# Kernel optimization log

Hardware: AMD Instinct MI355X
Metric: run time of the kernel (lower is better)

The kernel has to match this reference:

```python
import jax, jax.numpy as jnp
import numpy as np

EMBED_DIM = 1024
NUM_HEADS = 16
HEAD_DIM = EMBED_DIM // NUM_HEADS


def setup_inputs() -> dict:
    key = jax.random.key(0)
    ks = jax.random.split(key, 8)
    B, S, D = 4, 2048, EMBED_DIM
    scale = 1.0 / np.sqrt(D)
    return {
        "values": jax.random.normal(ks[0], (B, S, D), jnp.float32),
        "keys": jax.random.normal(ks[1], (B, S, D), jnp.float32),
        "query": jax.random.normal(ks[2], (B, S, D), jnp.float32),
        "Wv": jax.random.normal(ks[3], (D, D), jnp.float32) * scale,
        "Wk": jax.random.normal(ks[4], (D, D), jnp.float32) * scale,
        "Wq": jax.random.normal(ks[5], (D, D), jnp.float32) * scale,
        "Wo": jax.random.normal(ks[6], (D, D), jnp.float32) * scale,
        "bo": jnp.zeros((D,), jnp.float32),
    }


def reference(values, keys, query, Wv, Wk, Wq, Wo, bo):
    N = query.shape[0]
    H, Dh = NUM_HEADS, HEAD_DIM
    # torch Linear: x @ W.T  (weights stored [out, in])
    v = (values @ Wv.T).reshape(N, -1, H, Dh)
    k = (keys @ Wk.T).reshape(N, -1, H, Dh)
    q = (query @ Wq.T).reshape(N, -1, H, Dh)
    # energy: [N, H, q, k]
    energy = jnp.einsum("nqhd,nkhd->nhqk", q, k)
    # NOTE: original scales by sqrt(embed_dim), not sqrt(head_dim)
    attn = jax.nn.softmax(energy / jnp.sqrt(jnp.float32(EMBED_DIM)), axis=3)
    out = jnp.einsum("nhql,nlhd->nqhd", attn, v).reshape(N, -1, H * Dh)
    return out @ Wo.T + bo
```

## Files before the change

### kernel.cpp

```cpp
#include <hip/hip_runtime.h>
#include <stdint.h>

#define S_LEN   2048
#define D_MODEL 1024
#define N_HEADS 16
#define D_HEAD  64
#define BATCH   4
#define GM      8192
#define GN      1024
#define GK      1024
#define NKT     16

typedef __attribute__((ext_vector_type(8)))  short short8;
typedef __attribute__((ext_vector_type(4)))  short short4v;
typedef __attribute__((ext_vector_type(4)))  float f32x4;
typedef __attribute__((ext_vector_type(16))) float f32x16;

__device__ __forceinline__ short f2bf(float f) {
  unsigned u = __builtin_bit_cast(unsigned, f);
  u += 0x7fffu + ((u >> 16) & 1u);
  return (short)(u >> 16);
}

__device__ __forceinline__ unsigned cvt_pk_bf16(float lo, float hi) {
  unsigned r;
  asm("v_cvt_pk_bf16_f32 %0, %1, %2" : "=v"(r) : "v"(lo), "v"(hi));
  return r;
}

__device__ __forceinline__ short8 cvtf8(const float4 f0, const float4 f1) {
  unsigned u[4] = { cvt_pk_bf16(f0.x, f0.y), cvt_pk_bf16(f0.z, f0.w),
                    cvt_pk_bf16(f1.x, f1.y), cvt_pk_bf16(f1.z, f1.w) };
  return __builtin_bit_cast(short8, *(ulonglong2*)u);
}

__device__ __forceinline__ void gload_lds16(const short* g, short* lds_base) {
  __builtin_amdgcn_global_load_lds(
      (const __attribute__((address_space(1))) void*)(const void*)g,
      (__attribute__((address_space(3))) void*)(void*)lds_base, 16, 0, 0);
}

__global__ __launch_bounds__(256)
void cast_w(const float* __restrict__ W0, const float* __restrict__ W1,
            const float* __restrict__ W2, const float* __restrict__ W3,
            short* __restrict__ O0, short* __restrict__ O1,
            short* __restrict__ O2, short* __restrict__ O3)
{
  const int y = blockIdx.y;
  const float* src = (y == 0) ? W0 : (y == 1) ? W1 : (y == 2) ? W2 : W3;
  short*       dst = (y == 0) ? O0 : (y == 1) ? O1 : (y == 2) ? O2 : O3;
  const int gid = blockIdx.x * 256 + threadIdx.x;
  const int row = gid >> 7, gr = gid & 127;
  const int og  = (gr & ~7) | ((gr & 7) ^ (row & 7));
  const float* p = src + row * 1024 + gr * 8;
  short8 v = cvtf8(*(const float4*)p, *(const float4*)(p + 4));
  *(short8*)(dst + row * 1024 + og * 8) = v;
}

__global__ __launch_bounds__(256, 2)
void gemm_qkv(const float* __restrict__ Aq, const float* __restrict__ Ak,
              const float* __restrict__ Av,
              const short* __restrict__ Bq, const short* __restrict__ Bk,
              const short* __restrict__ Bv,
              short* __restrict__ Cq, short* __restrict__ Ck,
              short* __restrict__ Cv, float qscale)
{
  __shared__ short As[3 * 8192];
  __shared__ short Bs[2 * 8192];

  const int p  = blockIdx.x + (blockIdx.y << 3) + (blockIdx.z << 9);
  const int lg = (p & 7) * 192 + (p >> 3);
  const int z  = lg >> 9;
  const int by = (lg >> 3) & 63;
  const int bx = lg & 7;

  const float* Af = (z == 0) ? Aq : (z == 1) ? Ak : Av;
  const short* Bw = (z == 0) ? Bq : (z == 1) ? Bk : Bv;

  const int t = threadIdx.x;
  const int l = t & 63, w = t >> 6;
  const int lo = l & 15, g = l >> 4;
  const int wr = (w >> 1) * 64, wc = (w & 1) * 64;

  const int srow0 = w * 8 + (l >> 3);
  const int sg = l & 7;

  f32x4 acc[4][4] = {};
  float4 aA0[4], aA1[4], aB0[4], aB1[4];

  auto issueB = [&](int kt) {
#pragma unroll
    for (int i = 0; i < 4; ++i) {
      const int row = i * 32 + srow0;
      gload_lds16(Bw + (size_t)(bx * 128 + row) * GK + kt * 64 + sg * 8,
                  (short*)((char*)Bs + (kt & 1) * 16384 + i * 4096 + w * 1024));
    }
  };
  auto loadA = [&](int kt, float4 (&s0)[4], float4 (&s1)[4]) {
#pragma unroll
    for (int i = 0; i < 4; ++i) {
      const int row = i * 32 + srow0;
      const float* pa = Af + (size_t)(by * 128 + row) * GK + kt * 64 + sg * 8;
      s0[i] = *(const float4*)pa;
      s1[i] = *(const float4*)(pa + 4);
    }
  };
  auto writeA = [&](int kt, float4 (&s0)[4], float4 (&s1)[4]) {
    const int base = (kt % 3) * 8192;
#pragma unroll
    for (int i = 0; i < 4; ++i) {
      const int row = i * 32 + srow0;
      *(short8*)(&As[base + row * 64 + ((sg ^ (row & 7)) * 8)]) = cvtf8(s0[i], s1[i]);
    }
  };
  auto compute = [&](int it) {
    const int ab = (it % 3) * 8192;
    const int bb = (it & 1) * 8192;
#pragma unroll
    for (int kh = 0; kh < 2; ++kh) {
      short8 a[4], b[4];
      const int gg = ((kh * 4 + g) ^ (lo & 7)) * 8;
#pragma unroll
      for (int mi = 0; mi < 4; ++mi)
        a[mi] = *(const short8*)(&As[ab + (wr + mi * 16 + lo) * 64 + gg]);
#pragma unroll
      for (int ni = 0; ni < 4; ++ni)
        b[ni] = *(const short8*)(&Bs[bb + (wc + ni * 16 + lo) * 64 + gg]);
#pragma unroll
      for (int mi = 0; mi < 4; ++mi)
#pragma unroll
        for (int ni = 0; ni < 4; ++ni)
          acc[mi][ni] = __builtin_amdgcn_mfma_f32_16x16x32_bf16(a[mi], b[ni], acc[mi][ni], 0, 0, 0);
    }
  };

  auto halfIter = [&](int it, float4 (&ld0)[4], float4 (&ld1)[4],
                      float4 (&wr0)[4], float4 (&wr1)[4]) {
    if (it + 1 < NKT) issueB(it + 1);
    __builtin_amdgcn_sched_barrier(0);
    if (it + 2 < NKT) loadA(it + 2, ld0, ld1);
    compute(it);
    if (it + 1 < NKT) writeA(it + 1, wr0, wr1);
    if (it + 2 < NKT)
      asm volatile("s_waitcnt vmcnt(8) lgkmcnt(0)\n\ts_barrier" ::: "memory");
    else
      asm volatile("s_waitcnt vmcnt(0) lgkmcnt(0)\n\ts_barrier" ::: "memory");
  };

  loadA(0, aA0, aA1);
  issueB(0);
  writeA(0, aA0, aA1);
  loadA(1, aB0, aB1);
  asm volatile("s_waitcnt vmcnt(8) lgkmcnt(0)\n\ts_barrier" ::: "memory");

  for (int ith = 0; ith < NKT; ith += 2) {
    halfIter(ith,     aA0, aA1, aB0, aB1);
    halfIter(ith + 1, aB0, aB1, aA0, aA1);
  }

  const int rbase = by * 128 + wr + g * 4;
  const int cbase = bx * 128 + wc + lo;

  if (z < 2) {
    short* C = (z == 0) ? Cq : Ck;
    const float scale = (z == 0) ? qscale : 1.0f;
#pragma unroll
    for (int mi = 0; mi < 4; ++mi)
#pragma unroll
      for (int ni = 0; ni < 4; ++ni)
#pragma unroll
        for (int r = 0; r < 4; ++r)
          C[(size_t)(rbase + mi * 16 + r) * GN + cbase + ni * 16] = f2bf(acc[mi][ni][r] * scale);
  } else {
#pragma unroll
    for (int mi = 0; mi < 4; ++mi)
#pragma unroll
      for (int ni = 0; ni < 4; ++ni) {
        short4v v = {f2bf(acc[mi][ni][0]), f2bf(acc[mi][ni][1]),
                     f2bf(acc[mi][ni][2]), f2bf(acc[mi][ni][3])};
        *(short4v*)(&Cv[(size_t)(cbase + ni * 16) * GM + rbase + mi * 16]) = v;
      }
  }
}

__global__ __launch_bounds__(256, 2)
void gemm_out(const short* __restrict__ Ab, const short* __restrict__ Bw,
              float* __restrict__ C, const float* __restrict__ bias)
{
  __shared__ short As[2 * 8192];
  __shared__ short Bs[2 * 8192];

  const int p  = blockIdx.x + (blockIdx.y << 3);
  const int lg = (p & 7) * 64 + (p >> 3);
  const int by = lg >> 3;
  const int bx = lg & 7;

  const int t = threadIdx.x;
  const int l = t & 63, w = t >> 6;
  const int lo = l & 15, g = l >> 4;
  const int wr = (w >> 1) * 64, wc = (w & 1) * 64;

  const int srow0 = w * 8 + (l >> 3);
  const int sg = l & 7;

  f32x4 acc[4][4] = {};

#pragma unroll
  for (int i = 0; i < 4; ++i) {
    const int row = i * 32 + srow0;
    gload_lds16(Bw + (size_t)(bx * 128 + row) * GK + sg * 8,
                (short*)((char*)Bs + i * 4096 + w * 1024));
    gload_lds16(Ab + (size_t)(by * 128 + row) * GK + sg * 8,
                (short*)((char*)As + i * 4096 + w * 1024));
  }
  __syncthreads();

  for (int it = 0; it < NKT; ++it) {
    const int cur = it & 1;
    const int nxt = cur ^ 1;

    if (it + 1 < NKT) {
      const int kn = (it + 1) * 64;
#pragma unroll
      for (int i = 0; i < 4; ++i) {
        const int row = i * 32 + srow0;
        gload_lds16(Bw + (size_t)(bx * 128 + row) * GK + kn + sg * 8,
                    (short*)((char*)Bs + nxt * 16384 + i * 4096 + w * 1024));
        gload_lds16(Ab + (size_t)(by * 128 + row) * GK + kn + sg * 8,
                    (short*)((char*)As + nxt * 16384 + i * 4096 + w * 1024));
      }
    }

#pragma unroll
    for (int kh = 0; kh < 2; ++kh) {
      short8 a[4], b[4];
      const int gg = ((kh * 4 + g) ^ (lo & 7)) * 8;
#pragma unroll
      for (int mi = 0; mi < 4; ++mi)
        a[mi] = *(const short8*)(&As[cur * 8192 + (wr + mi * 16 + lo) * 64 + gg]);
#pragma unroll
      for (int ni = 0; ni < 4; ++ni)
        b[ni] = *(const short8*)(&Bs[cur * 8192 + (wc + ni * 16 + lo) * 64 + gg]);
#pragma unroll
      for (int mi = 0; mi < 4; ++mi)
#pragma unroll
        for (int ni = 0; ni < 4; ++ni)
          acc[mi][ni] = __builtin_amdgcn_mfma_f32_16x16x32_bf16(a[mi], b[ni], acc[mi][ni], 0, 0, 0);
    }
    __syncthreads();
  }

  const int rbase = by * 128 + wr + g * 4;
  const int cbase = bx * 128 + wc + lo;
#pragma unroll
  for (int ni = 0; ni < 4; ++ni) {
    const float bs = bias[cbase + ni * 16];
#pragma unroll
    for (int mi = 0; mi < 4; ++mi)
#pragma unroll
      for (int r = 0; r < 4; ++r)
        C[(size_t)(rbase + mi * 16 + r) * GN + cbase + ni * 16] = acc[mi][ni][r] + bs;
  }
}

__global__ __launch_bounds__(256, 3)
void attn_fwd4(const short* __restrict__ Q, const short* __restrict__ Kp,
               const short* __restrict__ Vt, short* __restrict__ O)
{
  __shared__ __align__(16) char smem[32768];

  const int bid = blockIdx.x;
  const int ol = ((bid & 7) << 7) | (bid >> 3);
  const int qt = ol & 15, h = (ol >> 4) & 15, n = ol >> 8;

  const int t = threadIdx.x, w = t >> 6, l = t & 63;
  const int lq = l & 31, hi = l >> 5;

  const short* qp = Q + ((size_t)(n * S_LEN + qt * 128 + w * 32 + lq)) * D_MODEL
                      + h * D_HEAD + hi * 8;
  short8 qf[4];
#pragma unroll
  for (int kc = 0; kc < 4; ++kc) qf[kc] = *(const short8*)(qp + kc * 16);

  const int srow = (w * 2) * 8 + (l >> 3);
  const int sg0  = (l & 7) ^ (srow & 7);
  const short* kstage = Kp + ((size_t)(n * S_LEN + srow)) * D_MODEL + h * D_HEAD + sg0 * 8;
  const short* vstage = Vt + ((size_t)(h * D_HEAD + srow)) * GM + (size_t)n * S_LEN + sg0 * 8;

  const int woff = (w * 2) * 1024;

  gload_lds16(kstage,               (short*)(smem + woff));
  gload_lds16(kstage + 8 * D_MODEL, (short*)(smem + woff + 1024));
  gload_lds16(vstage,               (short*)(smem + 16384 + woff));
  gload_lds16(vstage + 8 * GM,      (short*)(smem + 16384 + woff + 1024));
  __syncthreads();

  f32x16 oacc[2] = {};
  float lsum = 0.f;

  int cur = 0;
  for (int it = 0; it < S_LEN / 64; ++it) {
    const char* Kc = smem + cur * 8192;
    const char* Vc = smem + 16384 + cur * 8192;

    if (it + 1 < S_LEN / 64) {
      const int kvn = (it + 1) * 64;
      const int nxt = (cur ^ 1) * 8192;
      gload_lds16(kstage + (size_t)kvn * D_MODEL,       (short*)(smem + nxt + woff));
      gload_lds16(kstage + (size_t)(kvn + 8) * D_MODEL, (short*)(smem + nxt + woff + 1024));
      gload_lds16(vstage + kvn,                         (short*)(smem + 16384 + nxt + woff));
      gload_lds16(vstage + 8 * GM + kvn,                (short*)(smem + 16384 + nxt + woff + 1024));
    }

    f32x16 s0 = {}, s1 = {};
    __builtin_amdgcn_s_setprio(1);
#pragma unroll
    for (int kc = 0; kc < 4; ++kc) {
      const int r0 = lq, r1 = 32 + lq;
      const short8 k0 = *(const short8*)(Kc + r0 * 128 + (((kc * 2 + hi) ^ (r0 & 7)) << 4));
      const short8 k1 = *(const short8*)(Kc + r1 * 128 + (((kc * 2 + hi) ^ (r1 & 7)) << 4));
      s0 = __builtin_amdgcn_mfma_f32_32x32x16_bf16(k0, qf[kc], s0, 0, 0, 0);
      s1 = __builtin_amdgcn_mfma_f32_32x32x16_bf16(k1, qf[kc], s1, 0, 0, 0);
    }
    __builtin_amdgcn_s_setprio(0);

    float ps0 = 0.f, ps1 = 0.f, ps2 = 0.f, ps3 = 0.f;
    unsigned pk[16];
#pragma unroll
    for (int j = 0; j < 8; ++j) {
      const float p0 = __builtin_amdgcn_exp2f(s0[2 * j]);
      const float p1 = __builtin_amdgcn_exp2f(s0[2 * j + 1]);
      ps0 += p0; ps1 += p1;
      pk[j] = cvt_pk_bf16(p0, p1);
    }
#pragma unroll
    for (int j = 0; j < 8; ++j) {
      const float p0 = __builtin_amdgcn_exp2f(s1[2 * j]);
      const float p1 = __builtin_amdgcn_exp2f(s1[2 * j + 1]);
      ps2 += p0; ps3 += p1;
      pk[8 + j] = cvt_pk_bf16(p0, p1);
    }
    float psum = (ps0 + ps1) + (ps2 + ps3);
    psum += __shfl_xor(psum, 32, 64);
    lsum += psum;

    short8 pf[4];
#pragma unroll
    for (int kb = 0; kb < 2; ++kb)
#pragma unroll
      for (int ksl = 0; ksl < 2; ++ksl) {
        unsigned A0 = pk[kb * 8 + 4 * ksl];
        unsigned A1 = pk[kb * 8 + 4 * ksl + 1];
        unsigned B0 = pk[kb * 8 + 4 * ksl + 2];
        unsigned B1 = pk[kb * 8 + 4 * ksl + 3];
        asm("v_permlane32_swap_b32 %0, %1" : "+v"(A0), "+v"(B0));
        asm("v_permlane32_swap_b32 %0, %1" : "+v"(A1), "+v"(B1));
        unsigned wds[4] = {A0, A1, B0, B1};
        pf[kb * 2 + ksl] = __builtin_bit_cast(short8, *(ulonglong2*)wds);
      }

    __builtin_amdgcn_s_setprio(1);
#pragma unroll
    for (int dc = 0; dc < 2; ++dc)
#pragma unroll
      for (int ks = 0; ks < 4; ++ks) {
        const int rv = dc * 32 + lq;
        const short8 vfr = *(const short8*)(Vc + rv * 128 + (((ks * 2 + hi) ^ (rv & 7)) << 4));
        oacc[dc] = __builtin_amdgcn_mfma_f32_32x32x16_bf16(vfr, pf[ks], oacc[dc], 0, 0, 0);
      }
    __builtin_amdgcn_s_setprio(0);

    __syncthreads();
    cur ^= 1;
  }

  short (*Os)[32][72] = (short (*)[32][72])&smem[0];
  const float inv = __builtin_amdgcn_rcpf(lsum);
#pragma unroll
  for (int dc = 0; dc < 2; ++dc)
#pragma unroll
    for (int g = 0; g < 4; ++g) {
      const int d = 32 * dc + 8 * g + 4 * hi;
      short4v v = {f2bf(oacc[dc][4 * g] * inv),     f2bf(oacc[dc][4 * g + 1] * inv),
                   f2bf(oacc[dc][4 * g + 2] * inv), f2bf(oacc[dc][4 * g + 3] * inv)};
      *(short4v*)(&Os[w][lq][d]) = v;
    }

  const int ql = l >> 1, half = l & 1;
  short* op = O + ((size_t)(n * S_LEN + qt * 128 + w * 32 + ql)) * D_MODEL + h * D_HEAD;
#pragma unroll
  for (int j = 0; j < 4; ++j) {
    const int pg = (half * 4 + j) ^ (ql & 7);
    *(short8*)(op + pg * 8) = *(const short8*)(&Os[w][ql][half * 32 + j * 8]);
  }
}

extern "C" void kernel_launch(void* const* d_in, const int* in_sizes, int n_in,
                              void* d_out, int out_size, void* d_ws, size_t ws_size,
                              hipStream_t stream) {
  const float* values = (const float*)d_in[0];
  const float* keys   = (const float*)d_in[1];
  const float* query  = (const float*)d_in[2];
  const float* Wv     = (const float*)d_in[3];
  const float* Wk     = (const float*)d_in[4];
  const float* Wq     = (const float*)d_in[5];
  const float* Wo     = (const float*)d_in[6];
  const float* bo     = (const float*)d_in[7];
  float* out = (float*)d_out;

  short* wv = (short*)d_ws;
  short* wk = wv + (size_t)1024 * 1024;
  short* wq = wk + (size_t)1024 * 1024;
  short* wo = wq + (size_t)1024 * 1024;
  short* qp = wo + (size_t)1024 * 1024;
  short* kp = qp + (size_t)GM * GN;
  short* vt = kp + (size_t)GM * GN;
  short* ao = vt + (size_t)GM * GN;

  dim3 bb(256);
  const float qscale = 0.03125f * 1.44269504089f;

  cast_w<<<dim3(512, 4), bb, 0, stream>>>(Wv, Wk, Wq, Wo, wv, wk, wq, wo);

  gemm_qkv<<<dim3(GN / 128, GM / 128, 3), bb, 0, stream>>>(
      query, keys, values, wq, wk, wv, qp, kp, vt, qscale);

  attn_fwd4<<<dim3(S_LEN / 128 * N_HEADS * BATCH), bb, 0, stream>>>(qp, kp, vt, ao);

  gemm_out<<<dim3(GN / 128, GM / 128), bb, 0, stream>>>(ao, wo, out, bo);
}
```

Measured before the change: 189.1 us.

## Triple-buffer B tiles in output GEMM with partial vmcnt waits

The output projection GEMM now keeps three LDS buffers for the weight tile and two for the activation tile. It prefetches B two k-steps ahead and A one step ahead. The full __syncthreads is replaced with s_waitcnt vmcnt(4) plus s_barrier, so B loads can stay in flight across the barrier. LDS use grows from 64 KB to 80 KB per block, which may limit two blocks per CU. The change also depends on the order in which the vmcnt counters retire for correctness.

```diff
diff --git a/kernel.cpp b/kernel.cpp
--- a/kernel.cpp
+++ b/kernel.cpp
@@ -188,7 +188,7 @@
               float* __restrict__ C, const float* __restrict__ bias)
 {
   __shared__ short As[2 * 8192];
-  __shared__ short Bs[2 * 8192];
+  __shared__ short Bs[3 * 8192];
 
   const int p  = blockIdx.x + (blockIdx.y << 3);
   const int lg = (p & 7) * 64 + (p >> 3);
@@ -205,49 +205,55 @@
 
   f32x4 acc[4][4] = {};
 
-#pragma unroll
-  for (int i = 0; i < 4; ++i) {
-    const int row = i * 32 + srow0;
-    gload_lds16(Bw + (size_t)(bx * 128 + row) * GK + sg * 8,
-                (short*)((char*)Bs + i * 4096 + w * 1024));
-    gload_lds16(Ab + (size_t)(by * 128 + row) * GK + sg * 8,
-                (short*)((char*)As + i * 4096 + w * 1024));
-  }
-  __syncthreads();
+  auto issueA = [&](int kt) {
+#pragma unroll
+    for (int i = 0; i < 4; ++i) {
+      const int row = i * 32 + srow0;
+      gload_lds16(Ab + (size_t)(by * 128 + row) * GK + kt * 64 + sg * 8,
+                  (short*)((char*)As + (kt & 1) * 16384 + i * 4096 + w * 1024));
+    }
+  };
+  auto issueB = [&](int kt) {
+#pragma unroll
+    for (int i = 0; i < 4; ++i) {
+      const int row = i * 32 + srow0;
+      gload_lds16(Bw + (size_t)(bx * 128 + row) * GK + kt * 64 + sg * 8,
+                  (short*)((char*)Bs + (kt % 3) * 16384 + i * 4096 + w * 1024));
+    }
+  };
+
+  issueA(0);
+  issueB(0);
+  issueB(1);
+  asm volatile("s_waitcnt vmcnt(4) lgkmcnt(0)\n\ts_barrier" ::: "memory");
 
   for (int it = 0; it < NKT; ++it) {
-    const int cur = it & 1;
-    const int nxt = cur ^ 1;
-
-    if (it + 1 < NKT) {
-      const int kn = (it + 1) * 64;
-#pragma unroll
-      for (int i = 0; i < 4; ++i) {
-        const int row = i * 32 + srow0;
-        gload_lds16(Bw + (size_t)(bx * 128 + row) * GK + kn + sg * 8,
-                    (short*)((char*)Bs + nxt * 16384 + i * 4096 + w * 1024));
-        gload_lds16(Ab + (size_t)(by * 128 + row) * GK + kn + sg * 8,
-                    (short*)((char*)As + nxt * 16384 + i * 4096 + w * 1024));
-      }
-    }
-
+    if (it + 1 < NKT) issueA(it + 1);
+    if (it + 2 < NKT) issueB(it + 2);
+
+    const int ab = (it & 1) * 8192;
+    const int bb = (it % 3) * 8192;
 #pragma unroll
     for (int kh = 0; kh < 2; ++kh) {
       short8 a[4], b[4];
       const int gg = ((kh * 4 + g) ^ (lo & 7)) * 8;
 #pragma unroll
       for (int mi = 0; mi < 4; ++mi)
-        a[mi] = *(const short8*)(&As[cur * 8192 + (wr + mi * 16 + lo) * 64 + gg]);
+        a[mi] = *(const short8*)(&As[ab + (wr + mi * 16 + lo) * 64 + gg]);
 #pragma unroll
       for (int ni = 0; ni < 4; ++ni)
-        b[ni] = *(const short8*)(&Bs[cur * 8192 + (wc + ni * 16 + lo) * 64 + gg]);
+        b[ni] = *(const short8*)(&Bs[bb + (wc + ni * 16 + lo) * 64 + gg]);
 #pragma unroll
       for (int mi = 0; mi < 4; ++mi)
 #pragma unroll
         for (int ni = 0; ni < 4; ++ni)
           acc[mi][ni] = __builtin_amdgcn_mfma_f32_16x16x32_bf16(a[mi], b[ni], acc[mi][ni], 0, 0, 0);
     }
-    __syncthreads();
+
+    if (it + 2 < NKT)
+      asm volatile("s_waitcnt vmcnt(4) lgkmcnt(0)\n\ts_barrier" ::: "memory");
+    else
+      asm volatile("s_waitcnt vmcnt(0) lgkmcnt(0)\n\ts_barrier" ::: "memory");
   }
 
   const int rbase = by * 128 + wr + g * 4;
```

Result: no change. 191.2 us (+1.1%).
